# Performance work log

Hardware: AMD Instinct MI355X
Metric: run time of the kernel (lower is better)

The kernel has to match this reference:

```python
import jax, jax.numpy as jnp
import numpy as np

B, N, D = 16, 1024, 768
NEG = -1.0e9

def leaky_relu(x, slope=0.01):
    return jnp.where(x >= 0, x, slope * x)

def setup_inputs() -> dict:
    key = jax.random.key(0)
    ks = jax.random.split(key, 20)
    s = 0.02
    inp = {
        'inputs': jax.random.normal(ks[0], (B, N, D), dtype=jnp.float32),
        'adj_mat': jax.random.randint(ks[1], (B, N, N), 0, 2).astype(jnp.float32),
        # BaseGraphAttNet params
        'W_fc': jax.random.normal(ks[2], (D, D), dtype=jnp.float32) * s,
        'b_fc': jnp.zeros((D,), dtype=jnp.float32),
        'w_q': jax.random.normal(ks[3], (D,), dtype=jnp.float32) * s,
        'b_q': jnp.zeros((), dtype=jnp.float32),
        'w_k': jax.random.normal(ks[4], (D,), dtype=jnp.float32) * s,
        'b_k': jnp.zeros((), dtype=jnp.float32),
        # gating params (6 linears)
        'W_uy': jax.random.normal(ks[5], (D, D), dtype=jnp.float32) * s,
        'b_uy': jnp.zeros((D,), dtype=jnp.float32),
        'W_ux': jax.random.normal(ks[6], (D, D), dtype=jnp.float32) * s,
        'b_ux': jnp.zeros((D,), dtype=jnp.float32),
        'W_ry': jax.random.normal(ks[7], (D, D), dtype=jnp.float32) * s,
        'b_ry': jnp.zeros((D,), dtype=jnp.float32),
        'W_rx': jax.random.normal(ks[8], (D, D), dtype=jnp.float32) * s,
        'b_rx': jnp.zeros((D,), dtype=jnp.float32),
        'W_ty': jax.random.normal(ks[9], (D, D), dtype=jnp.float32) * s,
        'b_ty': jnp.zeros((D,), dtype=jnp.float32),
        'W_tx': jax.random.normal(ks[10], (D, D), dtype=jnp.float32) * s,
        'b_tx': jnp.zeros((D,), dtype=jnp.float32),
    }
    return inp

def reference(inputs, adj_mat, W_fc, b_fc, w_q, b_q, w_k, b_k,
              W_uy, b_uy, W_ux, b_ux, W_ry, b_ry, W_rx, b_rx,
              W_ty, b_ty, W_tx, b_tx):
    # ---- BaseGraphAttNet (residual=False); dropout in eval mode (identity) ----
    feat_proj = jnp.einsum('bnd,ed->bne', inputs, W_fc) + b_fc      # bs x N x D
    q = jnp.einsum('bnd,d->bn', feat_proj, w_q) + b_q               # bs x N
    k = jnp.einsum('bnd,d->bn', feat_proj, w_k) + b_k               # bs x N
    logits = q[:, :, None] + k[:, None, :]                          # bs x N x N
    masked = logits + (1.0 - adj_mat) * NEG
    masked = leaky_relu(masked)
    att = jax.nn.softmax(masked, axis=-1)
    y = jnp.einsum('bnm,bmd->bnd', att, feat_proj)                  # bs x N x D
    # ---- GRU-style gating ----
    u = jax.nn.sigmoid(jnp.einsum('bnd,ed->bne', y, W_uy) + b_uy
                       + jnp.einsum('bnd,ed->bne', inputs, W_ux) + b_ux)
    r = jax.nn.sigmoid(jnp.einsum('bnd,ed->bne', y, W_ry) + b_ry
                       + jnp.einsum('bnd,ed->bne', inputs, W_rx) + b_rx)
    x_tmp = jnp.tanh(jnp.einsum('bnd,ed->bne', y, W_ty) + b_ty
                     + jnp.einsum('bnd,ed->bne', r * inputs, W_tx) + b_tx)
    out = (1.0 - u) * inputs + u * x_tmp
    return out
```

## Files before the change

kernel.cpp:

```cpp
#include <hip/hip_runtime.h>
#include <cmath>

typedef __attribute__((ext_vector_type(8))) short bf16x8;
typedef __attribute__((ext_vector_type(4))) float f32x4;
typedef unsigned short u16;

struct __align__(8) us4 { u16 x, y, z, w; };

__device__ __forceinline__ u16 f2bf(float f) {
    union { float f; unsigned u; } v; v.f = f;
    unsigned u = v.u;
    u += 0x7fffu + ((u >> 16) & 1u);
    return (u16)(u >> 16);
}
__device__ __forceinline__ float bf2f(u16 h) {
    union { unsigned u; float f; } v; v.u = ((unsigned)h) << 16;
    return v.f;
}
__device__ __forceinline__ f32x4 mfma16(bf16x8 a, bf16x8 b, f32x4 c) {
    return __builtin_amdgcn_mfma_f32_16x16x32_bf16(a, b, c, 0, 0, 0);
}
__device__ __forceinline__ void ld_lds16(const u16* g, u16* l) {
    __builtin_amdgcn_global_load_lds(
        (const __attribute__((address_space(1))) unsigned int*)g,
        (__attribute__((address_space(3))) unsigned int*)l, 16, 0, 0);
}

__global__ __launch_bounds__(256) void cvtx(const float* __restrict__ in,
                                            u16* __restrict__ CatA, float* __restrict__ qkz) {
    int i = blockIdx.x * 256 + threadIdx.x;
    float4 f = reinterpret_cast<const float4*>(in)[i];
    us4 o; o.x = f2bf(f.x); o.y = f2bf(f.y); o.z = f2bf(f.z); o.w = f2bf(f.w);
    int row = i / 192, col = (i % 192) * 4;
    *reinterpret_cast<us4*>(CatA + (size_t)row * 1536 + 768 + col) = o;
    if (i < 8192) reinterpret_cast<float4*>(qkz)[i] = float4{0.f, 0.f, 0.f, 0.f};
}

struct WCvt { const float* s[7]; u16* d[7]; int ld[7]; };
__global__ __launch_bounds__(256) void cvtw(WCvt w) {
    int wi = blockIdx.y;
    int i = blockIdx.x * 256 + threadIdx.x;
    float4 f = reinterpret_cast<const float4*>(w.s[wi])[i];
    us4 o; o.x = f2bf(f.x); o.y = f2bf(f.y); o.z = f2bf(f.z); o.w = f2bf(f.w);
    int row = i / 192, col = (i % 192) * 4;
    *reinterpret_cast<us4*>(w.d[wi] + (size_t)row * w.ld[wi] + col) = o;
}

enum { EPI_FPT = 0, EPI_Y, EPI_GATES, EPI_OUT };

struct Epi {
    const float* b1; const float* b2; const float* b3; const float* b4;
    const float* wq; const float* wk; float* qv; float* kv;
    u16* fpT;
    u16* catA;
    const u16* xb;
    u16* ub_o; u16* rxb_o;
    const u16* ub; float* of;
};

template<int EPI, int PH>
__global__ __launch_bounds__(256) void g128(
    const u16* __restrict__ A1, const u16* __restrict__ B1,
    const u16* __restrict__ A2, const u16* __restrict__ B2,
    int K, int ldA1, int ldB1, int ldA2, int ldB2,
    size_t zA, size_t zB, Epi e)
{
    __shared__ __align__(16) u16 shm[17408];
    u16* const lA = shm;
    u16* const lB = shm + 8192;

    const int t = threadIdx.x;
    const int w = t >> 6, lane = t & 63, lm = lane & 15, quad = lane >> 4;
    const int row0 = blockIdx.x * 128;
    int col0, grp = 0;
    if constexpr (EPI == EPI_GATES) { grp = blockIdx.y / 6; col0 = (blockIdx.y % 6) * 128; }
    else col0 = blockIdx.y * 128;

    const int rs2 = t >> 3;
    const int kc2 = (((t & 7) ^ (rs2 & 7)) * 8);
    u16* dA_[4]; u16* dB_[4];
#pragma unroll
    for (int q = 0; q < 4; q++) {
        dA_[q] = lA + q * 2048 + w * 512;
        dB_[q] = lB + q * 2048 + w * 512;
    }

    const int rw0 = (w & 1) * 64, cw0 = (w >> 1) * 64;
    const int ch0 = ((quad) ^ (lm & 7)) * 8;
    const int ch1 = ((quad + 4) ^ (lm & 7)) * 8;
    int laB[4], lbB[4];
#pragma unroll
    for (int i = 0; i < 4; i++) laB[i] = (rw0 + i * 16 + lm) * 64;
#pragma unroll
    for (int j = 0; j < 4; j++) lbB[j] = (cw0 + j * 16 + lm) * 64;

    f32x4 acc[4][4] = {};
    bool first = true;

#pragma unroll
    for (int ph = 0; ph < PH; ph++) {
        const u16* As; const u16* Bs; int ldA, ldB;
        if (ph == 0) { As = A1 + (size_t)blockIdx.z * zA; Bs = B1 + (size_t)blockIdx.z * zB; ldA = ldA1; ldB = ldB1; }
        else         { As = A2; Bs = B2; ldA = ldA2; ldB = ldB2; }
        if constexpr (EPI == EPI_GATES) Bs += (size_t)grp * (768 * 1536);
        const u16* gA = As + (size_t)(row0 + rs2) * ldA + kc2;
        const u16* gB = Bs + (size_t)(col0 + rs2) * ldB + kc2;

        for (int k0 = 0; k0 < K; k0 += 64) {
            if (!first) __syncthreads();
            first = false;
#pragma unroll
            for (int q = 0; q < 4; q++) {
                ld_lds16(gA + (size_t)(q * 32) * ldA + k0, dA_[q]);
                ld_lds16(gB + (size_t)(q * 32) * ldB + k0, dB_[q]);
            }
            __syncthreads();

#pragma unroll
            for (int h = 0; h < 2; h++) {
                const int ch = h ? ch1 : ch0;
                bf16x8 a[4], b[4];
#pragma unroll
                for (int i = 0; i < 4; i++) a[i] = *reinterpret_cast<const bf16x8*>(lA + laB[i] + ch);
#pragma unroll
                for (int j = 0; j < 4; j++) b[j] = *reinterpret_cast<const bf16x8*>(lB + lbB[j] + ch);
#pragma unroll
                for (int i = 0; i < 4; i++)
#pragma unroll
                    for (int j = 0; j < 4; j++)
                        acc[i][j] = mfma16(a[i], b[j], acc[i][j]);
            }
        }
    }

    if constexpr (EPI == EPI_FPT) __syncthreads();

#pragma unroll
    for (int i = 0; i < 4; i++) {
        const int gr = row0 + rw0 + i * 16 + quad * 4;
        if constexpr (EPI == EPI_FPT) {
            float qp[4] = {}, kp[4] = {};
            const int nl = rw0 + i * 16 + quad * 4;
#pragma unroll
            for (int j = 0; j < 4; j++) {
                int gc = col0 + cw0 + j * 16 + lm;
                int dl = cw0 + j * 16 + lm;
                float bias = e.b1[gc];
                float v0 = acc[i][j][0] + bias, v1 = acc[i][j][1] + bias;
                float v2 = acc[i][j][2] + bias, v3 = acc[i][j][3] + bias;
                us4 o; o.x = f2bf(v0); o.y = f2bf(v1); o.z = f2bf(v2); o.w = f2bf(v3);
                *reinterpret_cast<us4*>(shm + dl * 136 + nl) = o;
                float wqv = e.wq[gc], wkv = e.wk[gc];
                qp[0] = fmaf(v0, wqv, qp[0]); qp[1] = fmaf(v1, wqv, qp[1]);
                qp[2] = fmaf(v2, wqv, qp[2]); qp[3] = fmaf(v3, wqv, qp[3]);
                kp[0] = fmaf(v0, wkv, kp[0]); kp[1] = fmaf(v1, wkv, kp[1]);
                kp[2] = fmaf(v2, wkv, kp[2]); kp[3] = fmaf(v3, wkv, kp[3]);
            }
#pragma unroll
            for (int r = 0; r < 4; r++) {
                float q = qp[r], k = kp[r];
#pragma unroll
                for (int m = 1; m < 16; m <<= 1) { q += __shfl_xor(q, m); k += __shfl_xor(k, m); }
                if (lm == 0) { atomicAdd(e.qv + gr + r, q); atomicAdd(e.kv + gr + r, k); }
            }
        } else if constexpr (EPI == EPI_Y) {
            size_t grow = (size_t)blockIdx.z * 1024 + gr;
#pragma unroll
            for (int j = 0; j < 4; j++) {
                int gc = col0 + cw0 + j * 16 + lm;
#pragma unroll
                for (int r = 0; r < 4; r++)
                    e.catA[(grow + r) * 1536 + gc] = f2bf(acc[i][j][r]);
            }
        } else if constexpr (EPI == EPI_GATES) {
#pragma unroll
            for (int j = 0; j < 4; j++) {
                int gc = col0 + cw0 + j * 16 + lm;
                if (grp == 0) {
                    float bias = e.b1[gc] + e.b2[gc];
#pragma unroll
                    for (int r = 0; r < 4; r++) {
                        size_t idx = (size_t)(gr + r) * 768 + gc;
                        e.ub_o[idx] = f2bf(1.f / (1.f + __expf(-(acc[i][j][r] + bias))));
                    }
                } else {
                    float bias = e.b3[gc] + e.b4[gc];
#pragma unroll
                    for (int r = 0; r < 4; r++) {
                        size_t idx = (size_t)(gr + r) * 768 + gc;
                        float rr = 1.f / (1.f + __expf(-(acc[i][j][r] + bias)));
                        float xv = bf2f(e.xb[(size_t)(gr + r) * 1536 + gc]);
                        e.rxb_o[idx] = f2bf(rr * xv);
                    }
                }
            }
        } else {
#pragma unroll
            for (int j = 0; j < 4; j++) {
                int gc = col0 + cw0 + j * 16 + lm;
                float bias = e.b1[gc] + e.b2[gc];
#pragma unroll
                for (int r = 0; r < 4; r++) {
                    size_t idx = (size_t)(gr + r) * 768 + gc;
                    float tt = tanhf(acc[i][j][r] + bias);
                    float uu = bf2f(e.ub[idx]);
                    float xv = bf2f(e.xb[(size_t)(gr + r) * 1536 + gc]);
                    e.of[idx] = (1.f - uu) * xv + uu * tt;
                }
            }
        }
    }

    if constexpr (EPI == EPI_FPT) {
        __syncthreads();
        const int bb = row0 >> 10, nn0 = row0 & 1023;
        const int dl = t >> 1, hf = t & 1;
        const u16* src = shm + dl * 136 + hf * 64;
        u16* dst = e.fpT + (size_t)bb * 786432 + (size_t)(col0 + dl) * 1024 + nn0 + hf * 64;
#pragma unroll
        for (int c = 0; c < 8; c++)
            *reinterpret_cast<bf16x8*>(dst + c * 8) =
                *reinterpret_cast<const bf16x8*>(src + c * 8);
    }
}

__global__ __launch_bounds__(256) void k_soft4(const float* __restrict__ adj,
                                               const float* __restrict__ qv,
                                               const float* __restrict__ kv,
                                               const float* __restrict__ bq,
                                               const float* __restrict__ bk,
                                               u16* __restrict__ attb) {
    int wv = threadIdx.x >> 6, lane = threadIdx.x & 63;
    int bn = blockIdx.x * 4 + wv;
    int b = bn >> 10;
    const float* adjrow = adj + (size_t)bn * 1024 + lane * 16;
    const float* krow = kv + (b << 10) + lane * 16;
    float q = qv[bn] + bq[0] + bk[0];

    float v[16];
#pragma unroll
    for (int c = 0; c < 4; c++) {
        float4 a4 = *reinterpret_cast<const float4*>(adjrow + c * 4);
        float4 k4 = *reinterpret_cast<const float4*>(krow + c * 4);
        float* vv = v + c * 4;
        vv[0] = q + k4.x + (1.f - a4.x) * -1.0e9f;
        vv[1] = q + k4.y + (1.f - a4.y) * -1.0e9f;
        vv[2] = q + k4.z + (1.f - a4.z) * -1.0e9f;
        vv[3] = q + k4.w + (1.f - a4.w) * -1.0e9f;
    }
#pragma unroll
    for (int t = 0; t < 16; t++) v[t] = v[t] >= 0.f ? v[t] : 0.01f * v[t];

    float mx = v[0];
#pragma unroll
    for (int t = 1; t < 16; t++) mx = fmaxf(mx, v[t]);
#pragma unroll
    for (int off = 32; off; off >>= 1) mx = fmaxf(mx, __shfl_xor(mx, off));

    float s = 0.f;
#pragma unroll
    for (int t = 0; t < 16; t++) { v[t] = __expf(v[t] - mx); s += v[t]; }
#pragma unroll
    for (int off = 32; off; off >>= 1) s += __shfl_xor(s, off);
    float inv = 1.f / s;

    u16* orow = attb + (size_t)bn * 1024 + lane * 16;
#pragma unroll
    for (int c = 0; c < 4; c++) {
        us4 o;
        o.x = f2bf(v[c * 4 + 0] * inv); o.y = f2bf(v[c * 4 + 1] * inv);
        o.z = f2bf(v[c * 4 + 2] * inv); o.w = f2bf(v[c * 4 + 3] * inv);
        *reinterpret_cast<us4*>(orow + c * 4) = o;
    }
}

extern "C" void kernel_launch(void* const* d_in, const int* in_sizes, int n_in,
                              void* d_out, int out_size, void* d_ws, size_t ws_size,
                              hipStream_t stream) {
    const float* x    = (const float*)d_in[0];
    const float* adj  = (const float*)d_in[1];
    const float* W_fc = (const float*)d_in[2];
    const float* b_fc = (const float*)d_in[3];
    const float* w_q  = (const float*)d_in[4];
    const float* b_q  = (const float*)d_in[5];
    const float* w_k  = (const float*)d_in[6];
    const float* b_k  = (const float*)d_in[7];
    const float* W_uy = (const float*)d_in[8];
    const float* b_uy = (const float*)d_in[9];
    const float* W_ux = (const float*)d_in[10];
    const float* b_ux = (const float*)d_in[11];
    const float* W_ry = (const float*)d_in[12];
    const float* b_ry = (const float*)d_in[13];
    const float* W_rx = (const float*)d_in[14];
    const float* b_rx = (const float*)d_in[15];
    const float* W_ty = (const float*)d_in[16];
    const float* b_ty = (const float*)d_in[17];
    const float* W_tx = (const float*)d_in[18];
    const float* b_tx = (const float*)d_in[19];

    char* ws = (char*)d_ws;
    u16*   CatA  = (u16*)  (ws + 0);
    u16*   Wfc_b = (u16*)  (ws + 50331648);
    u16*   Wty_b = (u16*)  (ws + 51511296);
    u16*   Wtx_b = (u16*)  (ws + 52690944);
    u16*   Wg    = (u16*)  (ws + 53870592);
    u16*   fpT   = (u16*)  (ws + 58589184);
    float* qv    = (float*)(ws + 83755008);
    float* kv    = (float*)(ws + 83820544);
    u16*   attb  = (u16*)  (ws + 83886080);
    u16*   u_b   = (u16*)  (ws + 83886080);
    u16*   rxb   = (u16*)  (ws + 117440512);

    cvtx<<<12288, 256, 0, stream>>>(x, CatA, qv);

    WCvt wc;
    wc.s[0] = W_fc; wc.d[0] = Wfc_b;              wc.ld[0] = 768;
    wc.s[1] = W_ty; wc.d[1] = Wty_b;              wc.ld[1] = 768;
    wc.s[2] = W_tx; wc.d[2] = Wtx_b;              wc.ld[2] = 768;
    wc.s[3] = W_uy; wc.d[3] = Wg;                 wc.ld[3] = 1536;
    wc.s[4] = W_ux; wc.d[4] = Wg + 768;           wc.ld[4] = 1536;
    wc.s[5] = W_ry; wc.d[5] = Wg + 768 * 1536;    wc.ld[5] = 1536;
    wc.s[6] = W_rx; wc.d[6] = Wg + 768 * 1536 + 768; wc.ld[6] = 1536;
    cvtw<<<dim3(576, 7), 256, 0, stream>>>(wc);

    Epi e{};
    e = Epi{}; e.b1 = b_fc; e.wq = w_q; e.wk = w_k; e.qv = qv; e.kv = kv; e.fpT = fpT;
    g128<EPI_FPT, 1><<<dim3(128, 6), 256, 0, stream>>>(CatA + 768, Wfc_b, nullptr, nullptr,
                                                       768, 1536, 768, 0, 0, 0, 0, e);

    k_soft4<<<4096, 256, 0, stream>>>(adj, qv, kv, b_q, b_k, attb);

    e = Epi{}; e.catA = CatA;
    g128<EPI_Y, 1><<<dim3(8, 6, 16), 256, 0, stream>>>(attb, fpT, nullptr, nullptr,
                                                       1024, 1024, 1024, 0, 0,
                                                       1048576, 786432, e);
    e = Epi{}; e.b1 = b_uy; e.b2 = b_ux; e.b3 = b_ry; e.b4 = b_rx;
    e.xb = CatA + 768; e.ub_o = u_b; e.rxb_o = rxb;
    g128<EPI_GATES, 1><<<dim3(128, 12), 256, 0, stream>>>(CatA, Wg, nullptr, nullptr,
                                                          1536, 1536, 1536, 0, 0, 0, 0, e);
    e = Epi{}; e.b1 = b_ty; e.b2 = b_tx; e.ub = u_b; e.xb = CatA + 768; e.of = (float*)d_out;
    g128<EPI_OUT, 2><<<dim3(128, 6), 256, 0, stream>>>(CatA, Wty_b, rxb, Wtx_b,
                                                       768, 1536, 768, 768, 768, 0, 0, e);
}
```

Baseline: 448.1 us.

## Rewrite GEMM as 256x128 tile, 8-wave, triple-buffered LDS pipeline

The 128x128 single-buffered GEMM is replaced by a 256x128 tile with 512 threads and a three-slot LDS ring that prefetches two K-tiles ahead. Compute is split into four MFMA phases, each interleaved with a slice of the next prefetch, using explicit vmcnt/lgkmcnt waits, raw barriers and s_setprio. The intent is to overlap global-to-LDS loads with MFMA work and raise reuse per tile. In exchange it uses far more LDS (about 144KB per block) and launches half as many blocks, which can hurt occupancy and tail balance.

```diff
diff --git a/kernel.cpp b/kernel.cpp
--- a/kernel.cpp
+++ b/kernel.cpp
@@ -25,6 +25,10 @@
         (const __attribute__((address_space(1))) unsigned int*)g,
         (__attribute__((address_space(3))) unsigned int*)l, 16, 0, 0);
 }
+
+#define VMCNT(n) asm volatile("s_waitcnt vmcnt(" #n ")" ::: "memory")
+#define LGKM0()  do { asm volatile("s_waitcnt lgkmcnt(0)" ::: "memory"); \
+                      __builtin_amdgcn_sched_barrier(0); } while (0)
 
 __global__ __launch_bounds__(256) void cvtx(const float* __restrict__ in,
                                             u16* __restrict__ CatA, float* __restrict__ qkz) {
@@ -58,34 +62,53 @@
     const u16* ub; float* of;
 };
 
-template<int EPI, int PH>
-__global__ __launch_bounds__(256) void g128(
-    const u16* __restrict__ A1, const u16* __restrict__ B1,
-    const u16* __restrict__ A2, const u16* __restrict__ B2,
-    int K, int ldA1, int ldB1, int ldA2, int ldB2,
-    size_t zA, size_t zB, Epi e)
-{
-    __shared__ __align__(16) u16 shm[17408];
-    u16* const lA = shm;
-    u16* const lB = shm + 8192;
+struct GArgs {
+    const u16 *A1, *B1, *A2, *B2;
+    int nt1, nt2, ldA1, ldB1, ldA2, ldB2;
+    size_t zA, zB;
+    Epi e;
+};
+
+template<int EPI>
+__device__ __forceinline__ void gk_body(const GArgs& g) {
+    __shared__ __align__(16) u16 lA[3 * 16384];
+    __shared__ __align__(16) u16 lB[3 * 8192];
 
     const int t = threadIdx.x;
     const int w = t >> 6, lane = t & 63, lm = lane & 15, quad = lane >> 4;
-    const int row0 = blockIdx.x * 128;
+    const int wm = w >> 1, wn = w & 1;
+    const int row0 = blockIdx.x * 256;
     int col0, grp = 0;
     if constexpr (EPI == EPI_GATES) { grp = blockIdx.y / 6; col0 = (blockIdx.y % 6) * 128; }
     else col0 = blockIdx.y * 128;
 
-    const int rs2 = t >> 3;
-    const int kc2 = (((t & 7) ^ (rs2 & 7)) * 8);
-    u16* dA_[4]; u16* dB_[4];
-#pragma unroll
-    for (int q = 0; q < 4; q++) {
-        dA_[q] = lA + q * 2048 + w * 512;
-        dB_[q] = lB + q * 2048 + w * 512;
-    }
-
-    const int rw0 = (w & 1) * 64, cw0 = (w >> 1) * 64;
+    const u16* A1p = g.A1 + (size_t)blockIdx.z * g.zA;
+    const u16* B1p = g.B1 + (size_t)blockIdx.z * g.zB;
+    if constexpr (EPI == EPI_GATES) B1p += (size_t)grp * (768 * 1536);
+    const int nt1 = g.nt1;
+    const int NT = g.nt1 + g.nt2;
+
+    const int srow = t >> 3;
+    const int scol = ((t & 7) ^ (srow & 7)) * 8;
+
+    auto stageA = [&](int ti, int slot, int u) {
+        const u16* S; int ld_, kk;
+        if (ti < nt1) { S = A1p; ld_ = g.ldA1; kk = ti * 64; }
+        else          { S = g.A2; ld_ = g.ldA2; kk = (ti - nt1) * 64; }
+        const u16* gp = S + (size_t)(row0 + u * 128 + srow) * ld_ + kk + scol;
+        u16* d = lA + slot * 16384 + u * 8192 + w * 512;
+        ld_lds16(gp, d);
+        ld_lds16(gp + (size_t)64 * ld_, d + 4096);
+    };
+    auto stageB = [&](int ti, int slot, int v) {
+        const u16* S; int ld_, kk;
+        if (ti < nt1) { S = B1p; ld_ = g.ldB1; kk = ti * 64; }
+        else          { S = g.B2; ld_ = g.ldB2; kk = (ti - nt1) * 64; }
+        const u16* gp = S + (size_t)(col0 + v * 64 + srow) * ld_ + kk + scol;
+        ld_lds16(gp, lB + slot * 8192 + v * 4096 + w * 512);
+    };
+
+    const int rw0 = wm * 64, cw0 = wn * 64;
     const int ch0 = ((quad) ^ (lm & 7)) * 8;
     const int ch1 = ((quad + 4) ^ (lm & 7)) * 8;
     int laB[4], lbB[4];
@@ -95,42 +118,80 @@
     for (int j = 0; j < 4; j++) lbB[j] = (cw0 + j * 16 + lm) * 64;
 
     f32x4 acc[4][4] = {};
-    bool first = true;
-
-#pragma unroll
-    for (int ph = 0; ph < PH; ph++) {
-        const u16* As; const u16* Bs; int ldA, ldB;
-        if (ph == 0) { As = A1 + (size_t)blockIdx.z * zA; Bs = B1 + (size_t)blockIdx.z * zB; ldA = ldA1; ldB = ldB1; }
-        else         { As = A2; Bs = B2; ldA = ldA2; ldB = ldB2; }
-        if constexpr (EPI == EPI_GATES) Bs += (size_t)grp * (768 * 1536);
-        const u16* gA = As + (size_t)(row0 + rs2) * ldA + kc2;
-        const u16* gB = Bs + (size_t)(col0 + rs2) * ldB + kc2;
-
-        for (int k0 = 0; k0 < K; k0 += 64) {
-            if (!first) __syncthreads();
-            first = false;
-#pragma unroll
-            for (int q = 0; q < 4; q++) {
-                ld_lds16(gA + (size_t)(q * 32) * ldA + k0, dA_[q]);
-                ld_lds16(gB + (size_t)(q * 32) * ldB + k0, dB_[q]);
-            }
-            __syncthreads();
-
-#pragma unroll
-            for (int h = 0; h < 2; h++) {
-                const int ch = h ? ch1 : ch0;
-                bf16x8 a[4], b[4];
-#pragma unroll
-                for (int i = 0; i < 4; i++) a[i] = *reinterpret_cast<const bf16x8*>(lA + laB[i] + ch);
-#pragma unroll
-                for (int j = 0; j < 4; j++) b[j] = *reinterpret_cast<const bf16x8*>(lB + lbB[j] + ch);
-#pragma unroll
-                for (int i = 0; i < 4; i++)
-#pragma unroll
-                    for (int j = 0; j < 4; j++)
-                        acc[i][j] = mfma16(a[i], b[j], acc[i][j]);
-            }
-        }
+
+    stageA(0, 0, 0); stageA(0, 0, 1); stageB(0, 0, 0); stageB(0, 0, 1);
+    stageA(1, 1, 0); stageA(1, 1, 1); stageB(1, 1, 0); stageB(1, 1, 1);
+    VMCNT(6);
+    __builtin_amdgcn_s_barrier();
+    __builtin_amdgcn_sched_barrier(0);
+
+    int scur = 0, spre = 2;
+    for (int T = 0; T < NT; ++T) {
+        const u16* bA = lA + scur * 16384;
+        const u16* bB = lB + scur * 8192;
+        const bool pf = (T + 2) < NT;
+        bf16x8 a0[4], a1[4], b0[4], b1[4];
+
+#pragma unroll
+        for (int i = 0; i < 4; i++) a0[i] = *reinterpret_cast<const bf16x8*>(bA + laB[i] + ch0);
+#pragma unroll
+        for (int j = 0; j < 4; j++) b0[j] = *reinterpret_cast<const bf16x8*>(bB + lbB[j] + ch0);
+        if (pf) stageA(T + 2, spre, 0);
+        __builtin_amdgcn_s_barrier();
+        LGKM0();
+        __builtin_amdgcn_s_setprio(1);
+#pragma unroll
+        for (int i = 0; i < 4; i++) {
+            acc[i][0] = mfma16(a0[i], b0[0], acc[i][0]);
+            acc[i][1] = mfma16(a0[i], b0[1], acc[i][1]);
+        }
+        __builtin_amdgcn_s_setprio(0);
+        __builtin_amdgcn_s_barrier();
+
+#pragma unroll
+        for (int i = 0; i < 4; i++) a1[i] = *reinterpret_cast<const bf16x8*>(bA + laB[i] + ch1);
+        if (pf) stageA(T + 2, spre, 1);
+        __builtin_amdgcn_s_barrier();
+        LGKM0();
+        __builtin_amdgcn_s_setprio(1);
+#pragma unroll
+        for (int i = 0; i < 4; i++) {
+            acc[i][2] = mfma16(a0[i], b0[2], acc[i][2]);
+            acc[i][3] = mfma16(a0[i], b0[3], acc[i][3]);
+        }
+        __builtin_amdgcn_s_setprio(0);
+        __builtin_amdgcn_s_barrier();
+
+#pragma unroll
+        for (int j = 0; j < 4; j++) b1[j] = *reinterpret_cast<const bf16x8*>(bB + lbB[j] + ch1);
+        if (pf) stageB(T + 2, spre, 0);
+        __builtin_amdgcn_s_barrier();
+        LGKM0();
+        __builtin_amdgcn_s_setprio(1);
+#pragma unroll
+        for (int i = 0; i < 4; i++) {
+            acc[i][0] = mfma16(a1[i], b1[0], acc[i][0]);
+            acc[i][1] = mfma16(a1[i], b1[1], acc[i][1]);
+        }
+        __builtin_amdgcn_s_setprio(0);
+        __builtin_amdgcn_s_barrier();
+
+        if (pf) stageB(T + 2, spre, 1);
+        __builtin_amdgcn_s_barrier();
+        LGKM0();
+        __builtin_amdgcn_s_setprio(1);
+#pragma unroll
+        for (int i = 0; i < 4; i++) {
+            acc[i][2] = mfma16(a1[i], b1[2], acc[i][2]);
+            acc[i][3] = mfma16(a1[i], b1[3], acc[i][3]);
+        }
+        __builtin_amdgcn_s_setprio(0);
+        if (T + 1 < NT) {
+            if (pf) { VMCNT(6); } else { VMCNT(0); }
+        }
+        __builtin_amdgcn_s_barrier();
+        scur = (scur == 2) ? 0 : scur + 1;
+        spre = (spre == 2) ? 0 : spre + 1;
     }
 
     if constexpr (EPI == EPI_FPT) __syncthreads();
@@ -145,12 +206,12 @@
             for (int j = 0; j < 4; j++) {
                 int gc = col0 + cw0 + j * 16 + lm;
                 int dl = cw0 + j * 16 + lm;
-                float bias = e.b1[gc];
+                float bias = g.e.b1[gc];
                 float v0 = acc[i][j][0] + bias, v1 = acc[i][j][1] + bias;
                 float v2 = acc[i][j][2] + bias, v3 = acc[i][j][3] + bias;
                 us4 o; o.x = f2bf(v0); o.y = f2bf(v1); o.z = f2bf(v2); o.w = f2bf(v3);
-                *reinterpret_cast<us4*>(shm + dl * 136 + nl) = o;
-                float wqv = e.wq[gc], wkv = e.wk[gc];
+                *reinterpret_cast<us4*>(lA + dl * 264 + nl) = o;
+                float wqv = g.e.wq[gc], wkv = g.e.wk[gc];
                 qp[0] = fmaf(v0, wqv, qp[0]); qp[1] = fmaf(v1, wqv, qp[1]);
                 qp[2] = fmaf(v2, wqv, qp[2]); qp[3] = fmaf(v3, wqv, qp[3]);
                 kp[0] = fmaf(v0, wkv, kp[0]); kp[1] = fmaf(v1, wkv, kp[1]);
@@ -161,7 +222,7 @@
                 float q = qp[r], k = kp[r];
 #pragma unroll
                 for (int m = 1; m < 16; m <<= 1) { q += __shfl_xor(q, m); k += __shfl_xor(k, m); }
-                if (lm == 0) { atomicAdd(e.qv + gr + r, q); atomicAdd(e.kv + gr + r, k); }
+                if (lm == 0) { atomicAdd(g.e.qv + gr + r, q); atomicAdd(g.e.kv + gr + r, k); }
             }
         } else if constexpr (EPI == EPI_Y) {
             size_t grow = (size_t)blockIdx.z * 1024 + gr;
@@ -170,27 +231,27 @@
                 int gc = col0 + cw0 + j * 16 + lm;
 #pragma unroll
                 for (int r = 0; r < 4; r++)
-                    e.catA[(grow + r) * 1536 + gc] = f2bf(acc[i][j][r]);
+                    g.e.catA[(grow + r) * 1536 + gc] = f2bf(acc[i][j][r]);
             }
         } else if constexpr (EPI == EPI_GATES) {
 #pragma unroll
             for (int j = 0; j < 4; j++) {
                 int gc = col0 + cw0 + j * 16 + lm;
                 if (grp == 0) {
-                    float bias = e.b1[gc] + e.b2[gc];
+                    float bias = g.e.b1[gc] + g.e.b2[gc];
 #pragma unroll
                     for (int r = 0; r < 4; r++) {
                         size_t idx = (size_t)(gr + r) * 768 + gc;
-                        e.ub_o[idx] = f2bf(1.f / (1.f + __expf(-(acc[i][j][r] + bias))));
+                        g.e.ub_o[idx] = f2bf(1.f / (1.f + __expf(-(acc[i][j][r] + bias))));
                     }
                 } else {
-                    float bias = e.b3[gc] + e.b4[gc];
+                    float bias = g.e.b3[gc] + g.e.b4[gc];
 #pragma unroll
                     for (int r = 0; r < 4; r++) {
                         size_t idx = (size_t)(gr + r) * 768 + gc;
                         float rr = 1.f / (1.f + __expf(-(acc[i][j][r] + bias)));
-                        float xv = bf2f(e.xb[(size_t)(gr + r) * 1536 + gc]);
-                        e.rxb_o[idx] = f2bf(rr * xv);
+                        float xv = bf2f(g.e.xb[(size_t)(gr + r) * 1536 + gc]);
+                        g.e.rxb_o[idx] = f2bf(rr * xv);
                     }
                 }
             }
@@ -198,14 +259,14 @@
 #pragma unroll
             for (int j = 0; j < 4; j++) {
                 int gc = col0 + cw0 + j * 16 + lm;
-                float bias = e.b1[gc] + e.b2[gc];
+                float bias = g.e.b1[gc] + g.e.b2[gc];
 #pragma unroll
                 for (int r = 0; r < 4; r++) {
                     size_t idx = (size_t)(gr + r) * 768 + gc;
-                    float tt = tanhf(acc[i][j][r] + bias);
-                    float uu = bf2f(e.ub[idx]);
-                    float xv = bf2f(e.xb[(size_t)(gr + r) * 1536 + gc]);
-                    e.of[idx] = (1.f - uu) * xv + uu * tt;
+                    float tv = tanhf(acc[i][j][r] + bias);
+                    float uu = bf2f(g.e.ub[idx]);
+                    float xv = bf2f(g.e.xb[(size_t)(gr + r) * 1536 + gc]);
+                    g.e.of[idx] = (1.f - uu) * xv + uu * tv;
                 }
             }
         }
@@ -214,15 +275,20 @@
     if constexpr (EPI == EPI_FPT) {
         __syncthreads();
         const int bb = row0 >> 10, nn0 = row0 & 1023;
-        const int dl = t >> 1, hf = t & 1;
-        const u16* src = shm + dl * 136 + hf * 64;
-        u16* dst = e.fpT + (size_t)bb * 786432 + (size_t)(col0 + dl) * 1024 + nn0 + hf * 64;
+        const int dl = t >> 2, seg = t & 3;
+        const u16* src = lA + dl * 264 + seg * 64;
+        u16* dst = g.e.fpT + (size_t)bb * 786432 + (size_t)(col0 + dl) * 1024 + nn0 + seg * 64;
 #pragma unroll
         for (int c = 0; c < 8; c++)
             *reinterpret_cast<bf16x8*>(dst + c * 8) =
                 *reinterpret_cast<const bf16x8*>(src + c * 8);
     }
 }
+
+__global__ __launch_bounds__(512, 2) void gFPT(GArgs g)   { gk_body<EPI_FPT>(g); }
+__global__ __launch_bounds__(512, 2) void gY(GArgs g)     { gk_body<EPI_Y>(g); }
+__global__ __launch_bounds__(512, 2) void gGATES(GArgs g) { gk_body<EPI_GATES>(g); }
+__global__ __launch_bounds__(512, 2) void gOUT(GArgs g)   { gk_body<EPI_OUT>(g); }
 
 __global__ __launch_bounds__(256) void k_soft4(const float* __restrict__ adj,
                                                const float* __restrict__ qv,
@@ -249,17 +315,17 @@
         vv[3] = q + k4.w + (1.f - a4.w) * -1.0e9f;
     }
 #pragma unroll
-    for (int t = 0; t < 16; t++) v[t] = v[t] >= 0.f ? v[t] : 0.01f * v[t];
+    for (int tt = 0; tt < 16; tt++) v[tt] = v[tt] >= 0.f ? v[tt] : 0.01f * v[tt];
 
     float mx = v[0];
 #pragma unroll
-    for (int t = 1; t < 16; t++) mx = fmaxf(mx, v[t]);
+    for (int tt = 1; tt < 16; tt++) mx = fmaxf(mx, v[tt]);
 #pragma unroll
     for (int off = 32; off; off >>= 1) mx = fmaxf(mx, __shfl_xor(mx, off));
 
     float s = 0.f;
 #pragma unroll
-    for (int t = 0; t < 16; t++) { v[t] = __expf(v[t] - mx); s += v[t]; }
+    for (int tt = 0; tt < 16; tt++) { v[tt] = __expf(v[tt] - mx); s += v[tt]; }
 #pragma unroll
     for (int off = 32; off; off >>= 1) s += __shfl_xor(s, off);
     float inv = 1.f / s;
@@ -324,21 +390,24 @@
     cvtw<<<dim3(576, 7), 256, 0, stream>>>(wc);
 
     Epi e{};
+    GArgs ga;
+
     e = Epi{}; e.b1 = b_fc; e.wq = w_q; e.wk = w_k; e.qv = qv; e.kv = kv; e.fpT = fpT;
-    g128<EPI_FPT, 1><<<dim3(128, 6), 256, 0, stream>>>(CatA + 768, Wfc_b, nullptr, nullptr,
-                                                       768, 1536, 768, 0, 0, 0, 0, e);
+    ga = GArgs{CatA + 768, Wfc_b, nullptr, nullptr, 12, 0, 1536, 768, 0, 0, 0, 0, e};
+    gFPT<<<dim3(64, 6), 512, 0, stream>>>(ga);
 
     k_soft4<<<4096, 256, 0, stream>>>(adj, qv, kv, b_q, b_k, attb);
 
     e = Epi{}; e.catA = CatA;
-    g128<EPI_Y, 1><<<dim3(8, 6, 16), 256, 0, stream>>>(attb, fpT, nullptr, nullptr,
-                                                       1024, 1024, 1024, 0, 0,
-                                                       1048576, 786432, e);
+    ga = GArgs{attb, fpT, nullptr, nullptr, 16, 0, 1024, 1024, 0, 0, 1048576, 786432, e};
+    gY<<<dim3(4, 6, 16), 512, 0, stream>>>(ga);
+
     e = Epi{}; e.b1 = b_uy; e.b2 = b_ux; e.b3 = b_ry; e.b4 = b_rx;
     e.xb = CatA + 768; e.ub_o = u_b; e.rxb_o = rxb;
-    g128<EPI_GATES, 1><<<dim3(128, 12), 256, 0, stream>>>(CatA, Wg, nullptr, nullptr,
-                                                          1536, 1536, 1536, 0, 0, 0, 0, e);
+    ga = GArgs{CatA, Wg, nullptr, nullptr, 24, 0, 1536, 1536, 0, 0, 0, 0, e};
+    gGATES<<<dim3(64, 12), 512, 0, stream>>>(ga);
+
     e = Epi{}; e.b1 = b_ty; e.b2 = b_tx; e.ub = u_b; e.xb = CatA + 768; e.of = (float*)d_out;
-    g128<EPI_OUT, 2><<<dim3(128, 6), 256, 0, stream>>>(CatA, Wty_b, rxb, Wtx_b,
-                                                       768, 1536, 768, 768, 768, 0, 0, e);
-}
+    ga = GArgs{CatA, Wty_b, rxb, Wtx_b, 12, 12, 1536, 768, 768, 768, 0, 0, e};
+    gOUT<<<dim3(64, 6), 512, 0, stream>>>(ga);
+}
```

New measurement: 538.4 us. +20.1%, slower.
